# Kernel optimization log

Measured on AMD Instinct MI355X. Metric: run time of the kernel, lower is better.

The kernel has to match this reference:

```python
import jax, jax.numpy as jnp
import numpy as np


def setup_inputs() -> dict:
    key = jax.random.key(0)
    # [batch, heads, seq, head_dim]
    hidden_states = jax.random.normal(key, (2, 16, 2048, 64), dtype=jnp.float32)
    return {"hidden_states": hidden_states}


def reference(hidden_states):
    q = k = v = hidden_states
    # scores: [b, h, s, s] -- note: NO 1/sqrt(d) scaling, matching the original.
    scores = jnp.einsum("bhqd,bhkd->bhqk", q, k)
    a = jax.nn.softmax(scores, axis=-1)
    out = jnp.einsum("bhqk,bhkd->bhqd", a, v)
    return out
```

## Files before the change

kernel.cpp:

```cpp
#include <hip/hip_runtime.h>
#include <hip/hip_bf16.h>
#include <stdint.h>


typedef __bf16 bf16x8 __attribute__((ext_vector_type(8)));
typedef __bf16 bf16x4 __attribute__((ext_vector_type(4)));
typedef __bf16 bf16x2 __attribute__((ext_vector_type(2)));
typedef float f32x4 __attribute__((ext_vector_type(4)));
typedef float f32x16 __attribute__((ext_vector_type(16)));
typedef unsigned int u32x4v __attribute__((ext_vector_type(4)));

#define SEQ 2048
#define HD 64
#define KVB 64
#define NBH 32
#define NTILE (SEQ / KVB)
#define IMG_BYTES 8192
#define PAIR_BYTES 16384
#define IMG_TOT ((size_t)NBH * NTILE * PAIR_BYTES)
#define WS_IMG IMG_TOT

#define QPB 128

__device__ __forceinline__ int swz(int row, int byteoff) {
    return byteoff ^ ((row & 7) << 4);
}

__device__ __forceinline__ float fexp2(float x) {
    float r;
    asm("v_exp_f32 %0, %1" : "=v"(r) : "v"(x));
    return r;
}

__device__ __forceinline__ unsigned pk_bf16(float a, float b) {
    bf16x2 v;
    v[0] = (__bf16)a;
    v[1] = (__bf16)b;
    return __builtin_bit_cast(unsigned, v);
}

__device__ __forceinline__ bf16x8 read_frag8(const char* base, int r, int p0) {
    const char* rowp = base + r * 128;
    const int rr = r & 15;
    bf16x4 lo = *(const bf16x4*)(rowp + (((p0 + 0) ^ rr) << 3));
    bf16x4 hi4 = *(const bf16x4*)(rowp + (((p0 + 1) ^ rr) << 3));
    bf16x8 f;
    f[0] = lo[0]; f[1] = lo[1]; f[2] = lo[2]; f[3] = lo[3];
    f[4] = hi4[0]; f[5] = hi4[1]; f[6] = hi4[2]; f[7] = hi4[3];
    return f;
}

#if __has_builtin(__builtin_amdgcn_global_load_lds)
#define HAVE_GLLDS 1
typedef const __attribute__((address_space(1))) unsigned int* gas_t;
typedef __attribute__((address_space(3))) unsigned int* las_t;
__device__ __forceinline__ void gl_lds16(const void* g, void* l) {
    __builtin_amdgcn_global_load_lds((gas_t)g, (las_t)l, 16, 0, 0);
}
#else
#define HAVE_GLLDS 0
#endif

__global__ __launch_bounds__(256)
void prep_kernel(const float* __restrict__ x, char* __restrict__ ws) {
    const int bh = blockIdx.y;
    const int tile = blockIdx.x;
    const int kv0 = tile * KVB;
    const int t = threadIdx.x;
    const int srow = t >> 2;
    const int scq = (t & 3) * 16;
    const float* __restrict__ X = x + (size_t)bh * SEQ * HD;
    char* __restrict__ img = ws + ((size_t)bh * NTILE + tile) * PAIR_BYTES;

    const int rr = srow & 15;
    const int p = scq >> 2;

    {
        const float* src = X + (size_t)(kv0 + srow) * HD + scq;
        float4 a = *(const float4*)(src);
        float4 b = *(const float4*)(src + 4);
        float4 c = *(const float4*)(src + 8);
        float4 d = *(const float4*)(src + 12);
        bf16x4 k0, k1, k2, k3;
        k0[0] = (__bf16)a.x; k0[1] = (__bf16)a.y; k0[2] = (__bf16)a.z; k0[3] = (__bf16)a.w;
        k1[0] = (__bf16)b.x; k1[1] = (__bf16)b.y; k1[2] = (__bf16)b.z; k1[3] = (__bf16)b.w;
        k2[0] = (__bf16)c.x; k2[1] = (__bf16)c.y; k2[2] = (__bf16)c.z; k2[3] = (__bf16)c.w;
        k3[0] = (__bf16)d.x; k3[1] = (__bf16)d.y; k3[2] = (__bf16)d.z; k3[3] = (__bf16)d.w;
        char* rowp = img + srow * 128;
        *(bf16x4*)(rowp + (((p + 0) ^ rr) << 3)) = k0;
        *(bf16x4*)(rowp + (((p + 1) ^ rr) << 3)) = k1;
        *(bf16x4*)(rowp + (((p + 2) ^ rr) << 3)) = k2;
        *(bf16x4*)(rowp + (((p + 3) ^ rr) << 3)) = k3;
    }
    {
        bf16x4 g0, g1, g2, g3;
#pragma unroll
        for (int j = 0; j < 4; ++j) {
            g0[j] = (__bf16)X[(size_t)(kv0 + scq + j) * HD + srow];
            g1[j] = (__bf16)X[(size_t)(kv0 + scq + 4 + j) * HD + srow];
            g2[j] = (__bf16)X[(size_t)(kv0 + scq + 8 + j) * HD + srow];
            g3[j] = (__bf16)X[(size_t)(kv0 + scq + 12 + j) * HD + srow];
        }
        char* rowp = img + IMG_BYTES + srow * 128;
        *(bf16x4*)(rowp + (((p + 0) ^ rr) << 3)) = g0;
        *(bf16x4*)(rowp + (((p + 1) ^ rr) << 3)) = g1;
        *(bf16x4*)(rowp + (((p + 2) ^ rr) << 3)) = g2;
        *(bf16x4*)(rowp + (((p + 3) ^ rr) << 3)) = g3;
    }
}

__global__ __launch_bounds__(256, 2)
void attn_img_kernel(const float* __restrict__ x, const char* __restrict__ ws,
                     float* __restrict__ outp) {
#if HAVE_GLLDS
    __shared__ __align__(16) char lds3[3][PAIR_BYTES];
#else
    __shared__ __align__(16) char lds3[2][PAIR_BYTES];
#endif

    const int wg = blockIdx.x;
    const int sid = (wg & 7) * 64 + (wg >> 3);
    const int bh = sid >> 4;
    const int q0 = (sid & 15) * QPB;

    const float* __restrict__ X = x + (size_t)bh * SEQ * HD;
    const char* __restrict__ wsb = ws + (size_t)bh * NTILE * PAIR_BYTES;

    const int t = threadIdx.x;
    const int wave = t >> 6;
    const int lane = t & 63;
    const int ln = lane & 31;
    const int hi = lane >> 5;

    const int qbase = q0 + wave * 32;

#if HAVE_GLLDS
    {
        const char* sp0 = wsb + wave * 4096 + lane * 16;
#pragma unroll
        for (int j = 0; j < 4; ++j)
            gl_lds16(sp0 + j * 1024, &lds3[0][wave * 4096 + j * 1024] + lane * 16);
        const char* sp1 = wsb + PAIR_BYTES + wave * 4096 + lane * 16;
#pragma unroll
        for (int j = 0; j < 4; ++j)
            gl_lds16(sp1 + j * 1024, &lds3[1][wave * 4096 + j * 1024] + lane * 16);
    }
#endif

    const float SCL = 1.4426950408889634f;
    bf16x8 qf[4];
    float m = 0.f;
    {
        const float* qsrc = X + (size_t)(qbase + ln) * HD;
#pragma unroll
        for (int j = 0; j < 16; ++j) {
            float4 v = *(const float4*)(qsrc + j * 4);
            m += v.x * v.x + v.y * v.y + v.z * v.z + v.w * v.w;
        }
        m *= SCL;
#pragma unroll
        for (int dt = 0; dt < 4; ++dt) {
            const float* s8 = qsrc + dt * 16 + hi * 8;
            float4 a = *(const float4*)s8;
            float4 b = *(const float4*)(s8 + 4);
            bf16x8 f;
            f[0] = (__bf16)(a.x * SCL); f[1] = (__bf16)(a.y * SCL);
            f[2] = (__bf16)(a.z * SCL); f[3] = (__bf16)(a.w * SCL);
            f[4] = (__bf16)(b.x * SCL); f[5] = (__bf16)(b.y * SCL);
            f[6] = (__bf16)(b.z * SCL); f[7] = (__bf16)(b.w * SCL);
            qf[dt] = f;
        }
    }

    f32x16 acc0, acc1;
#pragma unroll
    for (int i = 0; i < 16; ++i) { acc0[i] = 0.f; acc1[i] = 0.f; }
    float l = 0.f;

#if !HAVE_GLLDS
    {
        const char* img = wsb;
#pragma unroll
        for (int q = 0; q < 4; ++q) {
            bf16x8 d0 = *(const bf16x8*)(img + q * 4096 + t * 16);
            *(bf16x8*)&lds3[0][q * 4096 + t * 16] = d0;
        }
    }
    __syncthreads();
#endif

    for (int it = 0; it < NTILE; ++it) {
#if HAVE_GLLDS
        if (it + 1 < NTILE) {
            asm volatile("s_waitcnt vmcnt(4)" ::: "memory");
        } else {
            asm volatile("s_waitcnt vmcnt(0)" ::: "memory");
        }
        __builtin_amdgcn_s_barrier();
        __builtin_amdgcn_sched_barrier(0);

        if (it + 2 < NTILE) {
            const char* img = wsb + (size_t)(it + 2) * PAIR_BYTES;
            char* dst = &lds3[(it + 2) % 3][wave * 4096] + lane * 16;
            const char* sp = img + wave * 4096 + lane * 16;
#pragma unroll
            for (int j = 0; j < 4; ++j)
                gl_lds16(sp + j * 1024, dst + j * 1024);
        }
        const char* kb = lds3[it % 3];
#else
        bf16x8 n0, n1, n2, n3;
        if (it + 1 < NTILE) {
            const char* img = wsb + (size_t)(it + 1) * PAIR_BYTES;
            n0 = *(const bf16x8*)(img + t * 16);
            n1 = *(const bf16x8*)(img + 4096 + t * 16);
            n2 = *(const bf16x8*)(img + 8192 + t * 16);
            n3 = *(const bf16x8*)(img + 12288 + t * 16);
        }
        const char* kb = lds3[it & 1];
#endif
        const char* vb = kb + IMG_BYTES;

        f32x16 s0, s1;
#pragma unroll
        for (int i = 0; i < 16; ++i) { s0[i] = 0.f; s1[i] = 0.f; }
        __builtin_amdgcn_s_setprio(1);
#pragma unroll
        for (int dt = 0; dt < 4; ++dt) {
            const int p0 = dt * 4 + hi * 2;
            bf16x8 kf0 = read_frag8(kb, ln, p0);
            s0 = __builtin_amdgcn_mfma_f32_32x32x16_bf16(kf0, qf[dt], s0, 0, 0, 0);
            bf16x8 kf1 = read_frag8(kb, 32 + ln, p0);
            s1 = __builtin_amdgcn_mfma_f32_32x32x16_bf16(kf1, qf[dt], s1, 0, 0, 0);
        }
        __builtin_amdgcn_s_setprio(0);

        f32x16 e0, e1;
#pragma unroll
        for (int i = 0; i < 16; ++i) {
            e0[i] = fexp2(s0[i] - m);
            e1[i] = fexp2(s1[i] - m);
        }
        float ps = 0.f;
#pragma unroll
        for (int i = 0; i < 16; ++i) ps += e0[i] + e1[i];
        ps += __shfl_xor(ps, 32);
        l += ps;

        bf16x8 pa[4];
#pragma unroll
        for (int kt = 0; kt < 4; ++kt) {
            const f32x16& e = (kt & 2) ? e1 : e0;
            const int sx = 8 * (kt & 1);
            unsigned wA = pk_bf16(e[sx + 0], e[sx + 1]);
            unsigned wB = pk_bf16(e[sx + 2], e[sx + 3]);
            unsigned wC = pk_bf16(e[sx + 4], e[sx + 5]);
            unsigned wD = pk_bf16(e[sx + 6], e[sx + 7]);
            asm("v_permlane32_swap_b32 %0, %1" : "+v"(wA), "+v"(wC));
            asm("v_permlane32_swap_b32 %0, %1" : "+v"(wB), "+v"(wD));
            u32x4v w;
            w[0] = wA; w[1] = wB; w[2] = wC; w[3] = wD;
            pa[kt] = __builtin_bit_cast(bf16x8, w);
        }

        __builtin_amdgcn_s_setprio(1);
#pragma unroll
        for (int kt = 0; kt < 4; ++kt) {
            const int p0 = kt * 4 + hi * 2;
            bf16x8 vf0 = read_frag8(vb, ln, p0);
            acc0 = __builtin_amdgcn_mfma_f32_32x32x16_bf16(pa[kt], vf0, acc0, 0, 0, 0);
            bf16x8 vf1 = read_frag8(vb, 32 + ln, p0);
            acc1 = __builtin_amdgcn_mfma_f32_32x32x16_bf16(pa[kt], vf1, acc1, 0, 0, 0);
        }
        __builtin_amdgcn_s_setprio(0);

#if !HAVE_GLLDS
        if (it + 1 < NTILE) {
            const int nxt = (it + 1) & 1;
            __syncthreads();
            *(bf16x8*)&lds3[nxt][t * 16] = n0;
            *(bf16x8*)&lds3[nxt][4096 + t * 16] = n1;
            *(bf16x8*)&lds3[nxt][8192 + t * 16] = n2;
            *(bf16x8*)&lds3[nxt][12288 + t * 16] = n3;
            __syncthreads();
        }
#endif
    }

    float* Op = outp + (size_t)bh * SEQ * HD;
    const float invl = 1.f / l;
#pragma unroll
    for (int r = 0; r < 16; ++r) {
        const int qr = (r & 3) + 8 * (r >> 2) + 4 * hi;
        const float il = __shfl(invl, qr);
        float* dst = Op + (size_t)(qbase + qr) * HD + ln;
        dst[0]  = acc0[r] * il;
        dst[32] = acc1[r] * il;
    }
}

__global__ __launch_bounds__(256, 2)
void attn_fwd_kernel(const float* __restrict__ x, float* __restrict__ out) {
    __shared__ __align__(16) char k_lds[KVB * HD * 2];
    __shared__ __align__(16) char vt_lds[HD * KVB * 2];
    __shared__ __align__(16) char p_lds2[4][2][16 * KVB * 2];

    const int bh = blockIdx.y;
    const int q0 = blockIdx.x * 128;
    const float* __restrict__ X = x + (size_t)bh * SEQ * HD;
    float* __restrict__ Op = out + (size_t)bh * SEQ * HD;

    const int t = threadIdx.x;
    const int wave = t >> 6;
    const int lane = t & 63;
    const int lgrp = lane >> 4;
    const int lid = lane & 15;

    bf16x8 qf[2][2];
#pragma unroll
    for (int rt = 0; rt < 2; ++rt) {
        const int row = q0 + wave * 32 + rt * 16 + lid;
#pragma unroll
        for (int kc = 0; kc < 2; ++kc) {
            const float* src = X + (size_t)row * HD + kc * 32 + lgrp * 8;
            float4 a = *(const float4*)src;
            float4 b = *(const float4*)(src + 4);
            bf16x8 f;
            f[0] = (__bf16)a.x; f[1] = (__bf16)a.y; f[2] = (__bf16)a.z; f[3] = (__bf16)a.w;
            f[4] = (__bf16)b.x; f[5] = (__bf16)b.y; f[6] = (__bf16)b.z; f[7] = (__bf16)b.w;
            qf[rt][kc] = f;
        }
    }

    f32x4 acc[2][4];
    float m[2][4], l[2][4];
#pragma unroll
    for (int rt = 0; rt < 2; ++rt)
#pragma unroll
        for (int i = 0; i < 4; ++i) {
            acc[rt][i][0] = 0.f; acc[rt][i][1] = 0.f;
            acc[rt][i][2] = 0.f; acc[rt][i][3] = 0.f;
            m[rt][i] = -1e30f;
            l[rt][i] = 0.f;
        }

    const int srow = t >> 2;
    const int scq = (t & 3) * 16;

    for (int kv0 = 0; kv0 < SEQ; kv0 += KVB) {
        {
            const float* src = X + (size_t)(kv0 + srow) * HD + scq;
            float4 a = *(const float4*)(src);
            float4 b = *(const float4*)(src + 4);
            float4 c = *(const float4*)(src + 8);
            float4 d = *(const float4*)(src + 12);
            bf16x8 f0, f1;
            f0[0] = (__bf16)a.x; f0[1] = (__bf16)a.y; f0[2] = (__bf16)a.z; f0[3] = (__bf16)a.w;
            f0[4] = (__bf16)b.x; f0[5] = (__bf16)b.y; f0[6] = (__bf16)b.z; f0[7] = (__bf16)b.w;
            f1[0] = (__bf16)c.x; f1[1] = (__bf16)c.y; f1[2] = (__bf16)c.z; f1[3] = (__bf16)c.w;
            f1[4] = (__bf16)d.x; f1[5] = (__bf16)d.y; f1[6] = (__bf16)d.z; f1[7] = (__bf16)d.w;
            *(bf16x8*)&k_lds[swz(srow, srow * 128 + scq * 2)] = f0;
            *(bf16x8*)&k_lds[swz(srow, srow * 128 + scq * 2 + 16)] = f1;
        }
        {
            bf16x8 g0, g1;
#pragma unroll
            for (int j = 0; j < 8; ++j)
                g0[j] = (__bf16)X[(size_t)(kv0 + scq + j) * HD + srow];
#pragma unroll
            for (int j = 0; j < 8; ++j)
                g1[j] = (__bf16)X[(size_t)(kv0 + scq + 8 + j) * HD + srow];
            *(bf16x8*)&vt_lds[swz(srow, srow * 128 + scq * 2)] = g0;
            *(bf16x8*)&vt_lds[swz(srow, srow * 128 + scq * 2 + 16)] = g1;
        }
        __syncthreads();

#pragma unroll
        for (int rt = 0; rt < 2; ++rt) {
            f32x4 s[4];
#pragma unroll
            for (int kt = 0; kt < 4; ++kt) {
                f32x4 z = {0.f, 0.f, 0.f, 0.f};
#pragma unroll
                for (int kc = 0; kc < 2; ++kc) {
                    const int krow = kt * 16 + lid;
                    bf16x8 kfr = *(const bf16x8*)&k_lds[swz(krow, krow * 128 + (kc * 32 + lgrp * 8) * 2)];
                    z = __builtin_amdgcn_mfma_f32_16x16x32_bf16(qf[rt][kc], kfr, z, 0, 0, 0);
                }
                s[kt] = z;
            }

            char* pl = p_lds2[wave][rt];
#pragma unroll
            for (int r = 0; r < 4; ++r) {
                float mxv = fmaxf(fmaxf(s[0][r], s[1][r]), fmaxf(s[2][r], s[3][r]));
                mxv = fmaxf(mxv, __shfl_xor(mxv, 1));
                mxv = fmaxf(mxv, __shfl_xor(mxv, 2));
                mxv = fmaxf(mxv, __shfl_xor(mxv, 4));
                mxv = fmaxf(mxv, __shfl_xor(mxv, 8));
                const float mold = m[rt][r];
                const float mnew = fmaxf(mold, mxv);
                const float alpha = __expf(mold - mnew);
                const int prow = lgrp * 4 + r;
                float psum = 0.f;
#pragma unroll
                for (int kt = 0; kt < 4; ++kt) {
                    float p = __expf(s[kt][r] - mnew);
                    psum += p;
                    *(__bf16*)&pl[swz(prow, prow * 128 + (kt * 16 + lid) * 2)] = (__bf16)p;
                }
                psum += __shfl_xor(psum, 1);
                psum += __shfl_xor(psum, 2);
                psum += __shfl_xor(psum, 4);
                psum += __shfl_xor(psum, 8);
                l[rt][r] = l[rt][r] * alpha + psum;
                m[rt][r] = mnew;
#pragma unroll
                for (int ct = 0; ct < 4; ++ct)
                    acc[rt][ct][r] *= alpha;
            }

#pragma unroll
            for (int kc = 0; kc < 2; ++kc) {
                bf16x8 pfr = *(const bf16x8*)&pl[swz(lid, lid * 128 + (kc * 32 + lgrp * 8) * 2)];
#pragma unroll
                for (int ct = 0; ct < 4; ++ct) {
                    const int vrow = ct * 16 + lid;
                    bf16x8 vf = *(const bf16x8*)&vt_lds[swz(vrow, vrow * 128 + (kc * 32 + lgrp * 8) * 2)];
                    acc[rt][ct] = __builtin_amdgcn_mfma_f32_16x16x32_bf16(pfr, vf, acc[rt][ct], 0, 0, 0);
                }
            }
        }
        __syncthreads();
    }

#pragma unroll
    for (int rt = 0; rt < 2; ++rt)
#pragma unroll
        for (int r = 0; r < 4; ++r) {
            const float inv = 1.f / l[rt][r];
            const int row = q0 + wave * 32 + rt * 16 + lgrp * 4 + r;
            float* dst = Op + (size_t)row * HD + lid;
#pragma unroll
            for (int ct = 0; ct < 4; ++ct)
                dst[ct * 16] = acc[rt][ct][r] * inv;
        }
}

extern "C" void kernel_launch(void* const* d_in, const int* in_sizes, int n_in,
                              void* d_out, int out_size, void* d_ws, size_t ws_size,
                              hipStream_t stream) {
    const float* x = (const float*)d_in[0];
    float* out = (float*)d_out;
    char* ws = (char*)d_ws;
    if (ws_size >= WS_IMG) {
        dim3 pgrid(NTILE, NBH);
        hipLaunchKernelGGL(prep_kernel, pgrid, dim3(256), 0, stream, x, ws);
        hipLaunchKernelGGL(attn_img_kernel, dim3(512), dim3(256), 0, stream,
                           x, ws, out);
    } else {
        dim3 grid(SEQ / 128, NBH);
        hipLaunchKernelGGL(attn_fwd_kernel, grid, dim3(256), 0, stream, x, out);
    }
}
```

Measured before the change: 71.10 us.

## Software-pipeline QK^T of next tile with softmax and PV of current tile

Restructures the attention loop so the S=QK^T MFMAs for tile it+1 are issued before the exp/softmax and PV MFMAs of tile it. Two ping-pong score accumulators are used, and the loop is unrolled by two via a lambda. The prefetch is shifted to tile it+3 with a full vmcnt(0) wait plus a barrier at the end of each iteration. The non-GLLDS fallback path of the image kernel is removed. The aim is to overlap MFMA with the transcendental/VALU work, at the cost of more registers (two extra 32-float accumulators) and a stricter wait on global-to-LDS loads.

```diff
diff --git a/kernel.cpp b/kernel.cpp
--- a/kernel.cpp
+++ b/kernel.cpp
@@ -109,14 +109,11 @@
     }
 }
 
+#if HAVE_GLLDS
 __global__ __launch_bounds__(256, 2)
 void attn_img_kernel(const float* __restrict__ x, const char* __restrict__ ws,
                      float* __restrict__ outp) {
-#if HAVE_GLLDS
     __shared__ __align__(16) char lds3[3][PAIR_BYTES];
-#else
-    __shared__ __align__(16) char lds3[2][PAIR_BYTES];
-#endif
 
     const int wg = blockIdx.x;
     const int sid = (wg & 7) * 64 + (wg >> 3);
@@ -134,7 +131,6 @@
 
     const int qbase = q0 + wave * 32;
 
-#if HAVE_GLLDS
     {
         const char* sp0 = wsb + wave * 4096 + lane * 16;
 #pragma unroll
@@ -145,7 +141,6 @@
         for (int j = 0; j < 4; ++j)
             gl_lds16(sp1 + j * 1024, &lds3[1][wave * 4096 + j * 1024] + lane * 16);
     }
-#endif
 
     const float SCL = 1.4426950408889634f;
     bf16x8 qf[4];
@@ -177,69 +172,52 @@
     for (int i = 0; i < 16; ++i) { acc0[i] = 0.f; acc1[i] = 0.f; }
     float l = 0.f;
 
-#if !HAVE_GLLDS
-    {
-        const char* img = wsb;
-#pragma unroll
-        for (int q = 0; q < 4; ++q) {
-            bf16x8 d0 = *(const bf16x8*)(img + q * 4096 + t * 16);
-            *(bf16x8*)&lds3[0][q * 4096 + t * 16] = d0;
-        }
-    }
-    __syncthreads();
-#endif
-
-    for (int it = 0; it < NTILE; ++it) {
-#if HAVE_GLLDS
-        if (it + 1 < NTILE) {
-            asm volatile("s_waitcnt vmcnt(4)" ::: "memory");
-        } else {
-            asm volatile("s_waitcnt vmcnt(0)" ::: "memory");
-        }
-        __builtin_amdgcn_s_barrier();
-        __builtin_amdgcn_sched_barrier(0);
-
-        if (it + 2 < NTILE) {
-            const char* img = wsb + (size_t)(it + 2) * PAIR_BYTES;
-            char* dst = &lds3[(it + 2) % 3][wave * 4096] + lane * 16;
-            const char* sp = img + wave * 4096 + lane * 16;
-#pragma unroll
-            for (int j = 0; j < 4; ++j)
-                gl_lds16(sp + j * 1024, dst + j * 1024);
-        }
-        const char* kb = lds3[it % 3];
-#else
-        bf16x8 n0, n1, n2, n3;
-        if (it + 1 < NTILE) {
-            const char* img = wsb + (size_t)(it + 1) * PAIR_BYTES;
-            n0 = *(const bf16x8*)(img + t * 16);
-            n1 = *(const bf16x8*)(img + 4096 + t * 16);
-            n2 = *(const bf16x8*)(img + 8192 + t * 16);
-            n3 = *(const bf16x8*)(img + 12288 + t * 16);
-        }
-        const char* kb = lds3[it & 1];
-#endif
-        const char* vb = kb + IMG_BYTES;
-
-        f32x16 s0, s1;
-#pragma unroll
-        for (int i = 0; i < 16; ++i) { s0[i] = 0.f; s1[i] = 0.f; }
-        __builtin_amdgcn_s_setprio(1);
+    asm volatile("s_waitcnt vmcnt(0)" ::: "memory");
+    __builtin_amdgcn_s_barrier();
+    __builtin_amdgcn_sched_barrier(0);
+    {
+        const char* sp = wsb + (size_t)2 * PAIR_BYTES + wave * 4096 + lane * 16;
+        char* dst = &lds3[2][wave * 4096] + lane * 16;
+#pragma unroll
+        for (int j = 0; j < 4; ++j)
+            gl_lds16(sp + j * 1024, dst + j * 1024);
+    }
+
+    f32x16 sA0, sA1, sB0, sB1;
+    {
+        const char* kb = lds3[0];
+#pragma unroll
+        for (int i = 0; i < 16; ++i) { sA0[i] = 0.f; sA1[i] = 0.f; }
 #pragma unroll
         for (int dt = 0; dt < 4; ++dt) {
             const int p0 = dt * 4 + hi * 2;
             bf16x8 kf0 = read_frag8(kb, ln, p0);
-            s0 = __builtin_amdgcn_mfma_f32_32x32x16_bf16(kf0, qf[dt], s0, 0, 0, 0);
+            sA0 = __builtin_amdgcn_mfma_f32_32x32x16_bf16(kf0, qf[dt], sA0, 0, 0, 0);
             bf16x8 kf1 = read_frag8(kb, 32 + ln, p0);
-            s1 = __builtin_amdgcn_mfma_f32_32x32x16_bf16(kf1, qf[dt], s1, 0, 0, 0);
-        }
-        __builtin_amdgcn_s_setprio(0);
+            sA1 = __builtin_amdgcn_mfma_f32_32x32x16_bf16(kf1, qf[dt], sA1, 0, 0, 0);
+        }
+    }
+
+    auto iter_body = [&](int it, f32x16& c0, f32x16& c1, f32x16& n0, f32x16& n1) {
+        if (it + 1 < NTILE) {
+            const char* kb = lds3[(it + 1) % 3];
+#pragma unroll
+            for (int i = 0; i < 16; ++i) { n0[i] = 0.f; n1[i] = 0.f; }
+#pragma unroll
+            for (int dt = 0; dt < 4; ++dt) {
+                const int p0 = dt * 4 + hi * 2;
+                bf16x8 kf0 = read_frag8(kb, ln, p0);
+                n0 = __builtin_amdgcn_mfma_f32_32x32x16_bf16(kf0, qf[dt], n0, 0, 0, 0);
+                bf16x8 kf1 = read_frag8(kb, 32 + ln, p0);
+                n1 = __builtin_amdgcn_mfma_f32_32x32x16_bf16(kf1, qf[dt], n1, 0, 0, 0);
+            }
+        }
 
         f32x16 e0, e1;
 #pragma unroll
         for (int i = 0; i < 16; ++i) {
-            e0[i] = fexp2(s0[i] - m);
-            e1[i] = fexp2(s1[i] - m);
+            e0[i] = fexp2(c0[i] - m);
+            e1[i] = fexp2(c1[i] - m);
         }
         float ps = 0.f;
 #pragma unroll
@@ -263,6 +241,7 @@
             pa[kt] = __builtin_bit_cast(bf16x8, w);
         }
 
+        const char* vb = lds3[it % 3] + IMG_BYTES;
         __builtin_amdgcn_s_setprio(1);
 #pragma unroll
         for (int kt = 0; kt < 4; ++kt) {
@@ -274,17 +253,21 @@
         }
         __builtin_amdgcn_s_setprio(0);
 
-#if !HAVE_GLLDS
-        if (it + 1 < NTILE) {
-            const int nxt = (it + 1) & 1;
-            __syncthreads();
-            *(bf16x8*)&lds3[nxt][t * 16] = n0;
-            *(bf16x8*)&lds3[nxt][4096 + t * 16] = n1;
-            *(bf16x8*)&lds3[nxt][8192 + t * 16] = n2;
-            *(bf16x8*)&lds3[nxt][12288 + t * 16] = n3;
-            __syncthreads();
-        }
-#endif
+        asm volatile("s_waitcnt vmcnt(0)" ::: "memory");
+        __builtin_amdgcn_s_barrier();
+        __builtin_amdgcn_sched_barrier(0);
+        if (it + 3 < NTILE) {
+            const char* sp = wsb + (size_t)(it + 3) * PAIR_BYTES + wave * 4096 + lane * 16;
+            char* dst = &lds3[(it + 3) % 3][wave * 4096] + lane * 16;
+#pragma unroll
+            for (int j = 0; j < 4; ++j)
+                gl_lds16(sp + j * 1024, dst + j * 1024);
+        }
+    };
+
+    for (int it = 0; it < NTILE; it += 2) {
+        iter_body(it, sA0, sA1, sB0, sB1);
+        iter_body(it + 1, sB0, sB1, sA0, sA1);
     }
 
     float* Op = outp + (size_t)bh * SEQ * HD;
@@ -298,6 +281,7 @@
         dst[32] = acc1[r] * il;
     }
 }
+#endif
 
 __global__ __launch_bounds__(256, 2)
 void attn_fwd_kernel(const float* __restrict__ x, float* __restrict__ out) {
@@ -453,13 +437,15 @@
     const float* x = (const float*)d_in[0];
     float* out = (float*)d_out;
     char* ws = (char*)d_ws;
+#if HAVE_GLLDS
     if (ws_size >= WS_IMG) {
         dim3 pgrid(NTILE, NBH);
         hipLaunchKernelGGL(prep_kernel, pgrid, dim3(256), 0, stream, x, ws);
         hipLaunchKernelGGL(attn_img_kernel, dim3(512), dim3(256), 0, stream,
                            x, ws, out);
-    } else {
-        dim3 grid(SEQ / 128, NBH);
-        hipLaunchKernelGGL(attn_fwd_kernel, grid, dim3(256), 0, stream, x, out);
-    }
-}
+        return;
+    }
+#endif
+    dim3 grid(SEQ / 128, NBH);
+    hipLaunchKernelGGL(attn_fwd_kernel, grid, dim3(256), 0, stream, x, out);
+}
```

Result: slower. 160.1 us (+125.2%).
